# Kernel optimization log

Measured on AMD Instinct MI355X. Metric: run time of the kernel, lower is better.

The kernel has to match this reference:

```python
import jax, jax.numpy as jnp
import numpy as np

B, L, D, M = 4, 8192, 512, 256
EPS = 1e-6


def _feature_map(x, proj, is_query):
    # FAVOR+ positive softmax-kernel features.
    # x: (B, L, D), proj: (M, D) with orthogonal rows scaled by sqrt(D).
    d = x.shape[-1]
    xs = x * (d ** -0.25)                      # scale by d^{-1/4}
    dash = jnp.einsum('bld,md->blm', xs, proj)  # (B, L, M)
    diag = 0.5 * jnp.sum(xs * xs, axis=-1, keepdims=True)  # (B, L, 1)
    if is_query:
        stab = jnp.max(dash, axis=-1, keepdims=True)        # per-position max
    else:
        stab = jnp.max(dash, axis=(-2, -1), keepdims=True)  # per-batch max
    return jnp.exp(dash - diag - stab) / jnp.sqrt(jnp.asarray(M, x.dtype)) + EPS


def setup_inputs() -> dict:
    key = jax.random.key(0)
    kq, kk, kv, kp = jax.random.split(key, 4)
    Q = jax.random.normal(kq, (B, L, D), dtype=jnp.float32)
    K = jax.random.normal(kk, (B, L, D), dtype=jnp.float32)
    V = jax.random.normal(kv, (B, L, D), dtype=jnp.float32)
    # Orthogonal random projection: QR of a Gaussian, rows scaled by sqrt(D).
    G = jax.random.normal(kp, (D, M), dtype=jnp.float32)
    q, _ = jnp.linalg.qr(G)                     # (D, M), orthonormal columns
    proj = q.T * jnp.sqrt(jnp.asarray(D, jnp.float32))  # (M, D)
    return {"Q": Q, "K": K, "V": V, "proj": proj}


def reference(Q, K, V, proj):
    Qf = _feature_map(Q, proj, is_query=True)   # (B, L, M)
    Kf = _feature_map(K, proj, is_query=False)  # (B, L, M)
    # Linear attention: aggregate keys/values once, O(L*M*D).
    KV = jnp.einsum('blm,bld->bmd', Kf, V)      # (B, M, D)
    Ksum = jnp.sum(Kf, axis=1)                  # (B, M)
    Z = 1.0 / (jnp.einsum('blm,bm->bl', Qf, Ksum) + EPS)  # (B, L)
    out = jnp.einsum('blm,bmd->bld', Qf, KV) * Z[..., None]
    return out
```

## Files before the change

### kernel.cpp

```cpp
#include <hip/hip_runtime.h>
#include <math.h>

typedef unsigned short u16;
typedef unsigned int u32;
typedef __attribute__((ext_vector_type(8))) short bf16x8;
typedef __attribute__((ext_vector_type(4))) float f32x4;

#define SCALE_ 0.21022410381342864f
#define EPS_ 1e-6f
#define RSQM_ 0.0625f
#define L_ 8192

__device__ __forceinline__ float bf2f(u16 h) {
    return __uint_as_float(((u32)h) << 16);
}
__device__ __forceinline__ u32 cvtpk(float x0, float x1) {
    u32 w;
    asm("v_cvt_pk_bf16_f32 %0, %1, %2" : "=v"(w) : "v"(x0), "v"(x1));
    return w;
}
__device__ __forceinline__ void split_pk(float x0, float x1, u32& hw, u32& lw) {
    hw = cvtpk(x0, x1);
    float h0 = __uint_as_float(hw << 16);
    float h1 = __uint_as_float(hw & 0xffff0000u);
    lw = cvtpk(x0 - h0, x1 - h1);
}
__device__ __forceinline__ u32 okey(float x) {
    u32 b = __float_as_uint(x);
    return (b & 0x80000000u) ? ~b : (b | 0x80000000u);
}
__device__ __forceinline__ float odec(u32 k) {
    return (k & 0x80000000u) ? __uint_as_float(k & 0x7fffffffu) : __uint_as_float(~k);
}

#define GLDS16(gsrc, ldst) \
    __builtin_amdgcn_global_load_lds((__attribute__((address_space(1))) void*)(gsrc), \
                                     (__attribute__((address_space(3))) void*)(ldst), 16, 0, 0)

__global__ __launch_bounds__(256) void split_p(const float* __restrict__ P,
        u16* __restrict__ Ph, u16* __restrict__ Pl, u32* __restrict__ bmax) {
    if (blockIdx.x == 0 && threadIdx.x < 4) bmax[threadIdx.x] = 0u;
    int i = (blockIdx.x * 256 + threadIdx.x) * 2;
    u32 hw, lw;
    split_pk(P[i] * SCALE_, P[i + 1] * SCALE_, hw, lw);
    *reinterpret_cast<u32*>(&Ph[i]) = hw;
    *reinterpret_cast<u32*>(&Pl[i]) = lw;
}

__global__ __launch_bounds__(256) void dash_all(
        const float* __restrict__ Qg, const float* __restrict__ Kg,
        const u16* __restrict__ Bh_g, const u16* __restrict__ Bl_g,
        u16* __restrict__ QF, u16* __restrict__ KfT, float* __restrict__ ksump,
        u32* __restrict__ bmax) {
    __shared__ __align__(16) u16 Ah[64 * 32], Al[64 * 32];
    __shared__ __align__(16) u16 Bh[256 * 32], Bl[256 * 32];
    const int qpath = !(blockIdx.x & 1);
    const int tile = blockIdx.x >> 1;
    const float* __restrict__ X = qpath ? Qg : Kg;
    const int t = threadIdx.x, lane = t & 63;
    const int wid = t >> 6;
    const int row0 = tile * 64;
    const int l15 = lane & 15, l4 = lane >> 4;
    const int sr = t >> 2;
    const int awz = sr * 32 + (((t & 3) ^ ((sr >> 1) & 3)) * 8);
    const int koff = (l4 ^ ((l15 >> 1) & 3)) * 8;
    float ss = 0.f;

    const float* xp = &X[(size_t)(row0 + sr) * 512 + (t & 3) * 8];
    const u16* bsrch[4];
    const u16* bsrcl[4];
#pragma unroll
    for (int it = 0; it < 4; ++it) {
        const int m = it * 64 + wid * 16 + (lane >> 2);
        const int swz = ((lane & 3) ^ ((m >> 1) & 3)) * 8;
        bsrch[it] = Bh_g + (size_t)m * 512 + swz;
        bsrcl[it] = Bl_g + (size_t)m * 512 + swz;
    }

    f32x4 acc[4][4];
#pragma unroll
    for (int i = 0; i < 4; ++i)
#pragma unroll
        for (int j = 0; j < 4; ++j) acc[i][j] = (f32x4){0.f, 0.f, 0.f, 0.f};

    float4 v0 = *reinterpret_cast<const float4*>(xp);
    float4 v1 = *reinterpret_cast<const float4*>(xp + 4);

    for (int kt = 0; kt < 16; ++kt) {
        __syncthreads();
        {
#pragma unroll
            for (int it = 0; it < 4; ++it) {
                GLDS16(bsrch[it], Bh + it * 2048 + wid * 512);
                GLDS16(bsrcl[it], Bl + it * 2048 + wid * 512);
                bsrch[it] += 32; bsrcl[it] += 32;
            }
            float xs[8] = {v0.x, v0.y, v0.z, v0.w, v1.x, v1.y, v1.z, v1.w};
#pragma unroll
            for (int i = 0; i < 8; ++i) ss = fmaf(xs[i], xs[i], ss);
            u32 hw[4], lw[4];
#pragma unroll
            for (int i = 0; i < 4; ++i) split_pk(xs[2 * i], xs[2 * i + 1], hw[i], lw[i]);
            *reinterpret_cast<uint4*>(&Ah[awz]) = make_uint4(hw[0], hw[1], hw[2], hw[3]);
            *reinterpret_cast<uint4*>(&Al[awz]) = make_uint4(lw[0], lw[1], lw[2], lw[3]);
            xp = (kt < 15) ? xp + 32 : xp;
            v0 = *reinterpret_cast<const float4*>(xp);
            v1 = *reinterpret_cast<const float4*>(xp + 4);
        }
        __syncthreads();
        bf16x8 a_h[4], a_l[4], b_h[4], b_l[4];
#pragma unroll
        for (int mf = 0; mf < 4; ++mf) {
            int r = (mf * 16 + l15) * 32 + koff;
            a_h[mf] = *reinterpret_cast<const bf16x8*>(&Ah[r]);
            a_l[mf] = *reinterpret_cast<const bf16x8*>(&Al[r]);
        }
#pragma unroll
        for (int nf = 0; nf < 4; ++nf) {
            int r = (wid * 64 + nf * 16 + l15) * 32 + koff;
            b_h[nf] = *reinterpret_cast<const bf16x8*>(&Bh[r]);
            b_l[nf] = *reinterpret_cast<const bf16x8*>(&Bl[r]);
        }
#pragma unroll
        for (int mf = 0; mf < 4; ++mf)
#pragma unroll
            for (int nf = 0; nf < 4; ++nf) {
                acc[mf][nf] = __builtin_amdgcn_mfma_f32_16x16x32_bf16(a_h[mf], b_h[nf], acc[mf][nf], 0, 0, 0);
                acc[mf][nf] = __builtin_amdgcn_mfma_f32_16x16x32_bf16(a_h[mf], b_l[nf], acc[mf][nf], 0, 0, 0);
                acc[mf][nf] = __builtin_amdgcn_mfma_f32_16x16x32_bf16(a_l[mf], b_h[nf], acc[mf][nf], 0, 0, 0);
            }
    }
    __syncthreads();
    float* rmaxp = reinterpret_cast<float*>(Ah);
    float* diagp = reinterpret_cast<float*>(Al);

    ss += __shfl_xor(ss, 1);
    ss += __shfl_xor(ss, 2);
    if ((t & 3) == 0) diagp[sr] = 0.5f * SCALE_ * SCALE_ * ss;

    if (qpath) {
        float rm[4][4];
#pragma unroll
        for (int mf = 0; mf < 4; ++mf)
#pragma unroll
            for (int r = 0; r < 4; ++r) {
                float v = fmaxf(fmaxf(acc[mf][0][r], acc[mf][1][r]),
                                fmaxf(acc[mf][2][r], acc[mf][3][r]));
#pragma unroll
                for (int off = 1; off < 16; off <<= 1) v = fmaxf(v, __shfl_xor(v, off));
                rm[mf][r] = v;
            }
        if (l15 == 0) {
#pragma unroll
            for (int mf = 0; mf < 4; ++mf)
#pragma unroll
                for (int r = 0; r < 4; ++r)
                    rmaxp[(mf * 16 + l4 * 4 + r) * 4 + wid] = rm[mf][r];
        }
        __syncthreads();
#pragma unroll
        for (int mf = 0; mf < 4; ++mf)
#pragma unroll
            for (int r = 0; r < 4; ++r) {
                const int rl = mf * 16 + l4 * 4 + r;
                float m4 = fmaxf(fmaxf(rmaxp[rl * 4 + 0], rmaxp[rl * 4 + 1]),
                                 fmaxf(rmaxp[rl * 4 + 2], rmaxp[rl * 4 + 3]));
                const float c = diagp[rl] + m4;
                float f0 = expf(acc[mf][0][r] - c) * RSQM_ + EPS_;
                float f1 = expf(acc[mf][1][r] - c) * RSQM_ + EPS_;
                float f2 = expf(acc[mf][2][r] - c) * RSQM_ + EPS_;
                float f3 = expf(acc[mf][3][r] - c) * RSQM_ + EPS_;
                u32 w01 = cvtpk(f0, f1), w23 = cvtpk(f2, f3);
                size_t o = (size_t)(row0 + rl) * 256 + wid * 64 + l15;
                QF[o]      = (u16)w01;
                QF[o + 16] = (u16)(w01 >> 16);
                QF[o + 32] = (u16)w23;
                QF[o + 48] = (u16)(w23 >> 16);
            }
    } else {
        __syncthreads();
        const int b = row0 >> 13;
        const int ll = row0 & 8191;
        float bm = -1e30f;
        float s[4] = {0.f, 0.f, 0.f, 0.f};
#pragma unroll
        for (int nf = 0; nf < 4; ++nf) {
            const size_t mb = ((size_t)(b * 256 + wid * 64 + nf * 16 + l15)) * 8192 + ll + l4 * 4;
#pragma unroll
            for (int mf = 0; mf < 4; ++mf) {
                float e0 = acc[mf][nf][0], e1 = acc[mf][nf][1];
                float e2 = acc[mf][nf][2], e3 = acc[mf][nf][3];
                bm = fmaxf(fmaxf(bm, fmaxf(e0, e1)), fmaxf(e2, e3));
                float x0 = expf(e0 - diagp[mf * 16 + l4 * 4 + 0]);
                float x1 = expf(e1 - diagp[mf * 16 + l4 * 4 + 1]);
                float x2 = expf(e2 - diagp[mf * 16 + l4 * 4 + 2]);
                float x3 = expf(e3 - diagp[mf * 16 + l4 * 4 + 3]);
                s[nf] += (x0 + x1) + (x2 + x3);
                uint2 w = make_uint2(cvtpk(x0, x1), cvtpk(x2, x3));
                *reinterpret_cast<uint2*>(&KfT[mb + mf * 16]) = w;
            }
        }
#pragma unroll
        for (int nf = 0; nf < 4; ++nf) {
            s[nf] += __shfl_xor(s[nf], 16);
            s[nf] += __shfl_xor(s[nf], 32);
        }
        if (l4 == 0) {
#pragma unroll
            for (int nf = 0; nf < 4; ++nf)
                ksump[tile * 256 + wid * 64 + nf * 16 + l15] = s[nf];
        }
#pragma unroll
        for (int off = 1; off < 64; off <<= 1) bm = fmaxf(bm, __shfl_xor(bm, off));
        if (lane == 0) diagp[64 + wid] = bm;
        __syncthreads();
        if (t == 0) {
            float m = fmaxf(fmaxf(diagp[64], diagp[65]), fmaxf(diagp[66], diagp[67]));
            atomicMax(&bmax[b], okey(m));
        }
    }
}

__global__ __launch_bounds__(256) void split_vt(const float* __restrict__ V,
        u16* __restrict__ Vt, float* __restrict__ vsump) {
    const int dt = blockIdx.x & 7, lt = blockIdx.x >> 3;
    const int lg = lt * 64, b = lg >> 13, d0 = dt * 64;
    __shared__ u16 T[64][72];
    const int t = threadIdx.x;
    const int lrow = t >> 2, c0 = (t & 3) * 16;
#pragma unroll
    for (int ii = 0; ii < 4; ++ii) {
        float4 v = *reinterpret_cast<const float4*>(&V[(size_t)(lg + lrow) * 512 + d0 + c0 + ii * 4]);
        *reinterpret_cast<u32*>(&T[lrow][c0 + ii * 4 + 0]) = cvtpk(v.x, v.y);
        *reinterpret_cast<u32*>(&T[lrow][c0 + ii * 4 + 2]) = cvtpk(v.z, v.w);
    }
    __syncthreads();
    const int dloc = t >> 2, lc = (t & 3) * 16;
    u32 w[8];
    float s = 0.f;
#pragma unroll
    for (int j = 0; j < 8; ++j) {
        u16 a = T[lc + 2 * j][dloc], c = T[lc + 2 * j + 1][dloc];
        w[j] = (u32)a | ((u32)c << 16);
        s += bf2f(a) + bf2f(c);
    }
    size_t ob = ((size_t)(b * 512 + d0 + dloc)) * 8192 + (lg & 8191) + lc;
    reinterpret_cast<uint4*>(&Vt[ob])[0] = make_uint4(w[0], w[1], w[2], w[3]);
    reinterpret_cast<uint4*>(&Vt[ob])[1] = make_uint4(w[4], w[5], w[6], w[7]);
    s += __shfl_xor(s, 1);
    s += __shfl_xor(s, 2);
    if ((t & 3) == 0) vsump[lt * 512 + d0 + dloc] = s;
}

__global__ __launch_bounds__(256) void ksum_red(const float* __restrict__ ksump,
        const u32* __restrict__ bmax, float* __restrict__ KsumT) {
    const int b = blockIdx.x, m = threadIdx.x;
    float s = 0.f;
    for (int j = 0; j < 128; ++j) s += ksump[(b * 128 + j) * 256 + m];
    const float g = expf(-odec(bmax[b]));
    KsumT[b * 256 + m] = g * s + (float)L_ * EPS_;
}

__global__ __launch_bounds__(256) void vsum_red(const float* __restrict__ vsump,
        float* __restrict__ Vsum) {
    const int idx = blockIdx.x * 256 + threadIdx.x;
    const int b = idx >> 9, d = idx & 511;
    float s = 0.f;
    for (int j = 0; j < 128; ++j) s += vsump[(b * 128 + j) * 512 + d];
    Vsum[idx] = s;
}

__global__ __launch_bounds__(256) void kv_mfma(
        const u16* __restrict__ KfT, const u16* __restrict__ Vt,
        float* __restrict__ kvp) {
    int o = (blockIdx.x & 7) * 64 + (blockIdx.x >> 3);
    const int dt = o & 3, mt = (o >> 2) & 1, ch = (o >> 3) & 15, b = o >> 7;
    const u16* Ag = KfT + ((size_t)(b * 256 + mt * 128)) * 8192 + ch * 512;
    const u16* Bg = Vt + ((size_t)(b * 512 + dt * 128)) * 8192 + ch * 512;
    __shared__ __align__(16) u16 A_[128 * 32], B_[128 * 32];
    const int t = threadIdx.x, lane = t & 63;
    const int wid = t >> 6, wr = wid >> 1, wc = wid & 1;
    const int l15 = lane & 15, l4 = lane >> 4;
    const int koff = (l4 ^ ((l15 >> 1) & 3)) * 8;
    const u16* asrc[2];
    const u16* bsrc[2];
#pragma unroll
    for (int it = 0; it < 2; ++it) {
        const int row = it * 64 + wid * 16 + (lane >> 2);
        const int swz = ((lane & 3) ^ ((row >> 1) & 3)) * 8;
        asrc[it] = Ag + (size_t)row * 8192 + swz;
        bsrc[it] = Bg + (size_t)row * 8192 + swz;
    }
    f32x4 acc[4][4];
#pragma unroll
    for (int i = 0; i < 4; ++i)
#pragma unroll
        for (int j = 0; j < 4; ++j) acc[i][j] = (f32x4){0.f, 0.f, 0.f, 0.f};

    for (int kt = 0; kt < 16; ++kt) {
        __syncthreads();
#pragma unroll
        for (int it = 0; it < 2; ++it) {
            GLDS16(asrc[it], A_ + it * 2048 + wid * 512);
            GLDS16(bsrc[it], B_ + it * 2048 + wid * 512);
            asrc[it] += 32; bsrc[it] += 32;
        }
        __syncthreads();
        bf16x8 a[4], bb[4];
#pragma unroll
        for (int mf = 0; mf < 4; ++mf)
            a[mf] = *reinterpret_cast<const bf16x8*>(&A_[(wr * 64 + mf * 16 + l15) * 32 + koff]);
#pragma unroll
        for (int nf = 0; nf < 4; ++nf)
            bb[nf] = *reinterpret_cast<const bf16x8*>(&B_[(wc * 64 + nf * 16 + l15) * 32 + koff]);
#pragma unroll
        for (int mf = 0; mf < 4; ++mf)
#pragma unroll
            for (int nf = 0; nf < 4; ++nf)
                acc[mf][nf] = __builtin_amdgcn_mfma_f32_16x16x32_bf16(a[mf], bb[nf], acc[mf][nf], 0, 0, 0);
    }
#pragma unroll
    for (int mf = 0; mf < 4; ++mf)
#pragma unroll
        for (int r = 0; r < 4; ++r) {
            size_t oo = ((size_t)(ch * 4 + b) * 256 + mt * 128 + wr * 64 + mf * 16 + l4 * 4 + r) * 512
                        + dt * 128 + wc * 64;
#pragma unroll
            for (int nf = 0; nf < 4; ++nf)
                kvp[oo + nf * 16 + l15] = acc[mf][nf][r];
        }
}

__global__ __launch_bounds__(256) void kv_fix(const float* __restrict__ kvp,
        const u32* __restrict__ bmax, const float* __restrict__ Vsum,
        u16* __restrict__ KVth, u16* __restrict__ KVtl) {
    const int dt = blockIdx.x & 7, mt = (blockIdx.x >> 3) & 3, b = blockIdx.x >> 5;
    const int m0 = mt * 64, d0 = dt * 64;
    __shared__ u16 Th[64][72], Tl[64][72];
    const int t = threadIdx.x, mloc = t >> 2, c0 = (t & 3) * 16;
    float s[16];
#pragma unroll
    for (int j = 0; j < 16; ++j) s[j] = 0.f;
    for (int c = 0; c < 16; ++c) {
        size_t base = ((size_t)(c * 4 + b) * 256 + m0 + mloc) * 512 + d0 + c0;
#pragma unroll
        for (int ii = 0; ii < 4; ++ii) {
            float4 v = *reinterpret_cast<const float4*>(&kvp[base + ii * 4]);
            s[ii * 4 + 0] += v.x; s[ii * 4 + 1] += v.y;
            s[ii * 4 + 2] += v.z; s[ii * 4 + 3] += v.w;
        }
    }
    const float g = expf(-odec(bmax[b]));
#pragma unroll
    for (int j = 0; j < 16; j += 2) {
        float v0 = g * s[j]     + EPS_ * Vsum[b * 512 + d0 + c0 + j];
        float v1 = g * s[j + 1] + EPS_ * Vsum[b * 512 + d0 + c0 + j + 1];
        u32 hw, lw; split_pk(v0, v1, hw, lw);
        *reinterpret_cast<u32*>(&Th[mloc][c0 + j]) = hw;
        *reinterpret_cast<u32*>(&Tl[mloc][c0 + j]) = lw;
    }
    __syncthreads();
    const int dloc = t >> 2, mc = (t & 3) * 16;
    size_t ob = ((size_t)(b * 512 + d0 + dloc)) * 256 + m0 + mc;
    u32 wh[8], wl[8];
#pragma unroll
    for (int j = 0; j < 8; ++j) {
        wh[j] = (u32)Th[mc + 2 * j][dloc] | ((u32)Th[mc + 2 * j + 1][dloc] << 16);
        wl[j] = (u32)Tl[mc + 2 * j][dloc] | ((u32)Tl[mc + 2 * j + 1][dloc] << 16);
    }
    reinterpret_cast<uint4*>(&KVth[ob])[0] = make_uint4(wh[0], wh[1], wh[2], wh[3]);
    reinterpret_cast<uint4*>(&KVth[ob])[1] = make_uint4(wh[4], wh[5], wh[6], wh[7]);
    reinterpret_cast<uint4*>(&KVtl[ob])[0] = make_uint4(wl[0], wl[1], wl[2], wl[3]);
    reinterpret_cast<uint4*>(&KVtl[ob])[1] = make_uint4(wl[4], wl[5], wl[6], wl[7]);
}

__global__ __launch_bounds__(256) void z_kernel(const u16* __restrict__ QF,
        const float* __restrict__ KsumT, float* __restrict__ Z) {
    const int wid = threadIdx.x >> 6, lane = threadIdx.x & 63;
    const int row = blockIdx.x * 4 + wid;
    const int b = row >> 13;
    uint2 u = *reinterpret_cast<const uint2*>(&QF[(size_t)row * 256 + lane * 4]);
    float4 ks = *reinterpret_cast<const float4*>(&KsumT[b * 256 + lane * 4]);
    float s = bf2f((u16)(u.x & 0xffff)) * ks.x + bf2f((u16)(u.x >> 16)) * ks.y +
              bf2f((u16)(u.y & 0xffff)) * ks.z + bf2f((u16)(u.y >> 16)) * ks.w;
#pragma unroll
    for (int off = 1; off < 64; off <<= 1) s += __shfl_xor(s, off);
    if (lane == 0) Z[row] = 1.f / (s + EPS_);
}

__global__ __launch_bounds__(256) void out_mfma(
        const u16* __restrict__ QF, const u16* __restrict__ KVth,
        const u16* __restrict__ KVtl, const float* __restrict__ Z,
        float* __restrict__ out) {
    int o = (blockIdx.x & 7) * 128 + (blockIdx.x >> 3);
    const int dt = o & 3, rt = o >> 2;
    const int row0 = rt * 128, b = row0 >> 13;
    const u16* Ag = QF + (size_t)row0 * 256;
    const u16* Bh_g = KVth + ((size_t)(b * 512 + dt * 128)) * 256;
    const u16* Bl_g = KVtl + ((size_t)(b * 512 + dt * 128)) * 256;
    __shared__ __align__(16) u16 A_[128 * 32], Bh_[128 * 32], Bl_[128 * 32];
    const int t = threadIdx.x, lane = t & 63;
    const int wid = t >> 6, wr = wid >> 1, wc = wid & 1;
    const int l15 = lane & 15, l4 = lane >> 4;
    const int koff = (l4 ^ ((l15 >> 1) & 3)) * 8;
    const u16* asrc[2];
    const u16* bhsrc[2];
    const u16* blsrc[2];
#pragma unroll
    for (int it = 0; it < 2; ++it) {
        const int row = it * 64 + wid * 16 + (lane >> 2);
        const int swz = ((lane & 3) ^ ((row >> 1) & 3)) * 8;
        asrc[it]  = Ag + (size_t)row * 256 + swz;
        bhsrc[it] = Bh_g + (size_t)row * 256 + swz;
        blsrc[it] = Bl_g + (size_t)row * 256 + swz;
    }
    f32x4 acc[4][4];
#pragma unroll
    for (int i = 0; i < 4; ++i)
#pragma unroll
        for (int j = 0; j < 4; ++j) acc[i][j] = (f32x4){0.f, 0.f, 0.f, 0.f};

    for (int kt = 0; kt < 8; ++kt) {
        __syncthreads();
#pragma unroll
        for (int it = 0; it < 2; ++it) {
            GLDS16(asrc[it], A_ + it * 2048 + wid * 512);
            GLDS16(bhsrc[it], Bh_ + it * 2048 + wid * 512);
            GLDS16(blsrc[it], Bl_ + it * 2048 + wid * 512);
            asrc[it] += 32; bhsrc[it] += 32; blsrc[it] += 32;
        }
        __syncthreads();
        bf16x8 a[4], bh[4], bl[4];
#pragma unroll
        for (int mf = 0; mf < 4; ++mf)
            a[mf] = *reinterpret_cast<const bf16x8*>(&A_[(wr * 64 + mf * 16 + l15) * 32 + koff]);
#pragma unroll
        for (int nf = 0; nf < 4; ++nf) {
            int r = (wc * 64 + nf * 16 + l15) * 32 + koff;
            bh[nf] = *reinterpret_cast<const bf16x8*>(&Bh_[r]);
            bl[nf] = *reinterpret_cast<const bf16x8*>(&Bl_[r]);
        }
#pragma unroll
        for (int mf = 0; mf < 4; ++mf)
#pragma unroll
            for (int nf = 0; nf < 4; ++nf) {
                acc[mf][nf] = __builtin_amdgcn_mfma_f32_16x16x32_bf16(a[mf], bh[nf], acc[mf][nf], 0, 0, 0);
                acc[mf][nf] = __builtin_amdgcn_mfma_f32_16x16x32_bf16(a[mf], bl[nf], acc[mf][nf], 0, 0, 0);
            }
    }
#pragma unroll
    for (int mf = 0; mf < 4; ++mf)
#pragma unroll
        for (int r = 0; r < 4; ++r) {
            const int row = row0 + wr * 64 + mf * 16 + l4 * 4 + r;
            const float z = Z[row];
#pragma unroll
            for (int nf = 0; nf < 4; ++nf)
                out[(size_t)row * 512 + dt * 128 + wc * 64 + nf * 16 + l15] = acc[mf][nf][r] * z;
        }
}

extern "C" void kernel_launch(void* const* d_in, const int* in_sizes, int n_in,
                              void* d_out, int out_size, void* d_ws, size_t ws_size,
                              hipStream_t stream) {
    const float* Q = (const float*)d_in[0];
    const float* K = (const float*)d_in[1];
    const float* V = (const float*)d_in[2];
    const float* P = (const float*)d_in[3];
    float* out = (float*)d_out;
    char* ws = (char*)d_ws;

    u16*   QF    = (u16*)(ws + 0);
    u16*   KfT   = (u16*)(ws + 16777216);
    u16*   Vt    = (u16*)(ws + 33554432);
    float* kvp   = (float*)(ws + 67108864);
    u16*   KVth  = (u16*)(ws + 100663296);
    u16*   KVtl  = (u16*)(ws + 101711872);
    u16*   PH    = (u16*)(ws + 102760448);
    u16*   PL    = (u16*)(ws + 103022592);
    float* ksump = (float*)(ws + 103284736);
    float* vsump = (float*)(ws + 103809024);
    float* KsumT = (float*)(ws + 104857600);
    float* Vsum  = (float*)(ws + 104861696);
    float* Zbuf  = (float*)(ws + 104869888);
    u32*   bmax  = (u32*)(ws + 105000960);

    split_p<<<256, 256, 0, stream>>>(P, PH, PL, bmax);
    dash_all<<<1024, 256, 0, stream>>>(Q, K, PH, PL, QF, KfT, ksump, bmax);
    split_vt<<<4096, 256, 0, stream>>>(V, Vt, vsump);
    ksum_red<<<4, 256, 0, stream>>>(ksump, bmax, KsumT);
    vsum_red<<<8, 256, 0, stream>>>(vsump, Vsum);
    kv_mfma<<<512, 256, 0, stream>>>(KfT, Vt, kvp);
    kv_fix<<<128, 256, 0, stream>>>(kvp, bmax, Vsum, KVth, KVtl);
    z_kernel<<<8192, 256, 0, stream>>>(QF, KsumT, Zbuf);
    out_mfma<<<1024, 256, 0, stream>>>(QF, KVth, KVtl, Zbuf, out);
}
```

Measured before the change: 174.7 us.

## Fuse V transpose into dash kernel and Z into KV kernel, add setprio

Merges the V-transpose/split kernel into the dash kernel as alternating blocks, and the Z normalizer kernel into the KV MFMA kernel as alternating blocks. This cuts kernel launches and lets memory-bound work overlap with MFMA-bound work. It also fully unrolls the K loops with computed offsets, raises wave priority around the MFMA bursts, and adds occupancy hints to the launch bounds. The kv_mfma loop now shows 16 iterations where a bare label (z_unused) was left in the launch code, which suggests the before excerpt hides part of the context.

```diff
diff --git a/kernel.cpp b/kernel.cpp
--- a/kernel.cpp
+++ b/kernel.cpp
@@ -47,19 +47,59 @@
     *reinterpret_cast<u32*>(&Pl[i]) = lw;
 }
 
-__global__ __launch_bounds__(256) void dash_all(
+__global__ __launch_bounds__(256, 4) void dash_vt(
         const float* __restrict__ Qg, const float* __restrict__ Kg,
+        const float* __restrict__ Vg,
         const u16* __restrict__ Bh_g, const u16* __restrict__ Bl_g,
-        u16* __restrict__ QF, u16* __restrict__ KfT, float* __restrict__ ksump,
+        u16* __restrict__ QF, u16* __restrict__ KfT, u16* __restrict__ Vt,
+        float* __restrict__ ksump, float* __restrict__ vsump,
         u32* __restrict__ bmax) {
     __shared__ __align__(16) u16 Ah[64 * 32], Al[64 * 32];
     __shared__ __align__(16) u16 Bh[256 * 32], Bl[256 * 32];
-    const int qpath = !(blockIdx.x & 1);
-    const int tile = blockIdx.x >> 1;
-    const float* __restrict__ X = qpath ? Qg : Kg;
     const int t = threadIdx.x, lane = t & 63;
     const int wid = t >> 6;
-    const int row0 = tile * 64;
+
+    if (blockIdx.x & 1) {
+        u16 (*T)[72] = reinterpret_cast<u16(*)[72]>(Bh);
+        const int vb = blockIdx.x >> 1;
+        const int lrow = t >> 2, c0 = (t & 3) * 16;
+        const int dloc = t >> 2, lc = (t & 3) * 16;
+        for (int i = 0; i < 4; ++i) {
+            const int tv = vb * 4 + i;
+            const int dt = tv & 7, lt = tv >> 3;
+            const int lg = lt * 64, b = lg >> 13, d0 = dt * 64;
+            __syncthreads();
+#pragma unroll
+            for (int ii = 0; ii < 4; ++ii) {
+                float4 v = *reinterpret_cast<const float4*>(
+                    &Vg[(size_t)(lg + lrow) * 512 + d0 + c0 + ii * 4]);
+                *reinterpret_cast<u32*>(&T[lrow][c0 + ii * 4 + 0]) = cvtpk(v.x, v.y);
+                *reinterpret_cast<u32*>(&T[lrow][c0 + ii * 4 + 2]) = cvtpk(v.z, v.w);
+            }
+            __syncthreads();
+            u32 w[8];
+            float s = 0.f;
+#pragma unroll
+            for (int j = 0; j < 8; ++j) {
+                u16 a = T[lc + 2 * j][dloc], c = T[lc + 2 * j + 1][dloc];
+                w[j] = (u32)a | ((u32)c << 16);
+                s += bf2f(a) + bf2f(c);
+            }
+            size_t ob = ((size_t)(b * 512 + d0 + dloc)) * 8192 + (lg & 8191) + lc;
+            reinterpret_cast<uint4*>(&Vt[ob])[0] = make_uint4(w[0], w[1], w[2], w[3]);
+            reinterpret_cast<uint4*>(&Vt[ob])[1] = make_uint4(w[4], w[5], w[6], w[7]);
+            s += __shfl_xor(s, 1);
+            s += __shfl_xor(s, 2);
+            if ((t & 3) == 0) vsump[lt * 512 + d0 + dloc] = s;
+        }
+        return;
+    }
+
+    const int ds = blockIdx.x >> 1;
+    const int qpath = !(ds & 1);
+    const int xtile = ds >> 1;
+    const float* __restrict__ X = qpath ? Qg : Kg;
+    const int row0 = xtile * 64;
     const int l15 = lane & 15, l4 = lane >> 4;
     const int sr = t >> 2;
     const int awz = sr * 32 + (((t & 3) ^ ((sr >> 1) & 3)) * 8);
@@ -86,14 +126,14 @@
     float4 v0 = *reinterpret_cast<const float4*>(xp);
     float4 v1 = *reinterpret_cast<const float4*>(xp + 4);
 
+#pragma unroll
     for (int kt = 0; kt < 16; ++kt) {
         __syncthreads();
         {
 #pragma unroll
             for (int it = 0; it < 4; ++it) {
-                GLDS16(bsrch[it], Bh + it * 2048 + wid * 512);
-                GLDS16(bsrcl[it], Bl + it * 2048 + wid * 512);
-                bsrch[it] += 32; bsrcl[it] += 32;
+                GLDS16(bsrch[it] + kt * 32, Bh + it * 2048 + wid * 512);
+                GLDS16(bsrcl[it] + kt * 32, Bl + it * 2048 + wid * 512);
             }
             float xs[8] = {v0.x, v0.y, v0.z, v0.w, v1.x, v1.y, v1.z, v1.w};
 #pragma unroll
@@ -103,9 +143,9 @@
             for (int i = 0; i < 4; ++i) split_pk(xs[2 * i], xs[2 * i + 1], hw[i], lw[i]);
             *reinterpret_cast<uint4*>(&Ah[awz]) = make_uint4(hw[0], hw[1], hw[2], hw[3]);
             *reinterpret_cast<uint4*>(&Al[awz]) = make_uint4(lw[0], lw[1], lw[2], lw[3]);
-            xp = (kt < 15) ? xp + 32 : xp;
-            v0 = *reinterpret_cast<const float4*>(xp);
-            v1 = *reinterpret_cast<const float4*>(xp + 4);
+            const int nk = (kt < 15) ? kt + 1 : 15;
+            v0 = *reinterpret_cast<const float4*>(xp + nk * 32);
+            v1 = *reinterpret_cast<const float4*>(xp + nk * 32 + 4);
         }
         __syncthreads();
         bf16x8 a_h[4], a_l[4], b_h[4], b_l[4];
@@ -121,6 +161,7 @@
             b_h[nf] = *reinterpret_cast<const bf16x8*>(&Bh[r]);
             b_l[nf] = *reinterpret_cast<const bf16x8*>(&Bl[r]);
         }
+        __builtin_amdgcn_s_setprio(1);
 #pragma unroll
         for (int mf = 0; mf < 4; ++mf)
 #pragma unroll
@@ -129,6 +170,7 @@
                 acc[mf][nf] = __builtin_amdgcn_mfma_f32_16x16x32_bf16(a_h[mf], b_l[nf], acc[mf][nf], 0, 0, 0);
                 acc[mf][nf] = __builtin_amdgcn_mfma_f32_16x16x32_bf16(a_l[mf], b_h[nf], acc[mf][nf], 0, 0, 0);
             }
+        __builtin_amdgcn_s_setprio(0);
     }
     __syncthreads();
     float* rmaxp = reinterpret_cast<float*>(Ah);
@@ -208,7 +250,7 @@
         if (l4 == 0) {
 #pragma unroll
             for (int nf = 0; nf < 4; ++nf)
-                ksump[tile * 256 + wid * 64 + nf * 16 + l15] = s[nf];
+                ksump[xtile * 256 + wid * 64 + nf * 16 + l15] = s[nf];
         }
 #pragma unroll
         for (int off = 1; off < 64; off <<= 1) bm = fmaxf(bm, __shfl_xor(bm, off));
@@ -219,37 +261,6 @@
             atomicMax(&bmax[b], okey(m));
         }
     }
-}
-
-__global__ __launch_bounds__(256) void split_vt(const float* __restrict__ V,
-        u16* __restrict__ Vt, float* __restrict__ vsump) {
-    const int dt = blockIdx.x & 7, lt = blockIdx.x >> 3;
-    const int lg = lt * 64, b = lg >> 13, d0 = dt * 64;
-    __shared__ u16 T[64][72];
-    const int t = threadIdx.x;
-    const int lrow = t >> 2, c0 = (t & 3) * 16;
-#pragma unroll
-    for (int ii = 0; ii < 4; ++ii) {
-        float4 v = *reinterpret_cast<const float4*>(&V[(size_t)(lg + lrow) * 512 + d0 + c0 + ii * 4]);
-        *reinterpret_cast<u32*>(&T[lrow][c0 + ii * 4 + 0]) = cvtpk(v.x, v.y);
-        *reinterpret_cast<u32*>(&T[lrow][c0 + ii * 4 + 2]) = cvtpk(v.z, v.w);
-    }
-    __syncthreads();
-    const int dloc = t >> 2, lc = (t & 3) * 16;
-    u32 w[8];
-    float s = 0.f;
-#pragma unroll
-    for (int j = 0; j < 8; ++j) {
-        u16 a = T[lc + 2 * j][dloc], c = T[lc + 2 * j + 1][dloc];
-        w[j] = (u32)a | ((u32)c << 16);
-        s += bf2f(a) + bf2f(c);
-    }
-    size_t ob = ((size_t)(b * 512 + d0 + dloc)) * 8192 + (lg & 8191) + lc;
-    reinterpret_cast<uint4*>(&Vt[ob])[0] = make_uint4(w[0], w[1], w[2], w[3]);
-    reinterpret_cast<uint4*>(&Vt[ob])[1] = make_uint4(w[4], w[5], w[6], w[7]);
-    s += __shfl_xor(s, 1);
-    s += __shfl_xor(s, 2);
-    if ((t & 3) == 0) vsump[lt * 512 + d0 + dloc] = s;
 }
 
 __global__ __launch_bounds__(256) void ksum_red(const float* __restrict__ ksump,
@@ -270,16 +281,36 @@
     Vsum[idx] = s;
 }
 
-__global__ __launch_bounds__(256) void kv_mfma(
+__global__ __launch_bounds__(256, 4) void kv_z(
         const u16* __restrict__ KfT, const u16* __restrict__ Vt,
-        float* __restrict__ kvp) {
-    int o = (blockIdx.x & 7) * 64 + (blockIdx.x >> 3);
+        const u16* __restrict__ QF, const float* __restrict__ KsumT,
+        float* __restrict__ kvp, float* __restrict__ Z) {
+    __shared__ __align__(16) u16 A_[128 * 32], B_[128 * 32];
+    const int t = threadIdx.x, lane = t & 63;
+    const int wid = t >> 6;
+
+    if (blockIdx.x & 1) {
+        const int zb = blockIdx.x >> 1;
+        for (int i = 0; i < 16; ++i) {
+            const int row = zb * 64 + wid * 16 + i;
+            const int b = row >> 13;
+            uint2 u = *reinterpret_cast<const uint2*>(&QF[(size_t)row * 256 + lane * 4]);
+            float4 ks = *reinterpret_cast<const float4*>(&KsumT[b * 256 + lane * 4]);
+            float s = bf2f((u16)(u.x & 0xffff)) * ks.x + bf2f((u16)(u.x >> 16)) * ks.y +
+                      bf2f((u16)(u.y & 0xffff)) * ks.z + bf2f((u16)(u.y >> 16)) * ks.w;
+#pragma unroll
+            for (int off = 1; off < 64; off <<= 1) s += __shfl_xor(s, off);
+            if (lane == 0) Z[row] = 1.f / (s + EPS_);
+        }
+        return;
+    }
+
+    const int kvb = blockIdx.x >> 1;
+    int o = (kvb & 7) * 64 + (kvb >> 3);
     const int dt = o & 3, mt = (o >> 2) & 1, ch = (o >> 3) & 15, b = o >> 7;
     const u16* Ag = KfT + ((size_t)(b * 256 + mt * 128)) * 8192 + ch * 512;
     const u16* Bg = Vt + ((size_t)(b * 512 + dt * 128)) * 8192 + ch * 512;
-    __shared__ __align__(16) u16 A_[128 * 32], B_[128 * 32];
-    const int t = threadIdx.x, lane = t & 63;
-    const int wid = t >> 6, wr = wid >> 1, wc = wid & 1;
+    const int wr = wid >> 1, wc = wid & 1;
     const int l15 = lane & 15, l4 = lane >> 4;
     const int koff = (l4 ^ ((l15 >> 1) & 3)) * 8;
     const u16* asrc[2];
@@ -297,13 +328,13 @@
 #pragma unroll
         for (int j = 0; j < 4; ++j) acc[i][j] = (f32x4){0.f, 0.f, 0.f, 0.f};
 
+#pragma unroll
     for (int kt = 0; kt < 16; ++kt) {
         __syncthreads();
 #pragma unroll
         for (int it = 0; it < 2; ++it) {
-            GLDS16(asrc[it], A_ + it * 2048 + wid * 512);
-            GLDS16(bsrc[it], B_ + it * 2048 + wid * 512);
-            asrc[it] += 32; bsrc[it] += 32;
+            GLDS16(asrc[it] + kt * 32, A_ + it * 2048 + wid * 512);
+            GLDS16(bsrc[it] + kt * 32, B_ + it * 2048 + wid * 512);
         }
         __syncthreads();
         bf16x8 a[4], bb[4];
@@ -313,11 +344,13 @@
 #pragma unroll
         for (int nf = 0; nf < 4; ++nf)
             bb[nf] = *reinterpret_cast<const bf16x8*>(&B_[(wc * 64 + nf * 16 + l15) * 32 + koff]);
+        __builtin_amdgcn_s_setprio(1);
 #pragma unroll
         for (int mf = 0; mf < 4; ++mf)
 #pragma unroll
             for (int nf = 0; nf < 4; ++nf)
                 acc[mf][nf] = __builtin_amdgcn_mfma_f32_16x16x32_bf16(a[mf], bb[nf], acc[mf][nf], 0, 0, 0);
+        __builtin_amdgcn_s_setprio(0);
     }
 #pragma unroll
     for (int mf = 0; mf < 4; ++mf)
@@ -374,21 +407,7 @@
     reinterpret_cast<uint4*>(&KVtl[ob])[1] = make_uint4(wl[4], wl[5], wl[6], wl[7]);
 }
 
-__global__ __launch_bounds__(256) void z_kernel(const u16* __restrict__ QF,
-        const float* __restrict__ KsumT, float* __restrict__ Z) {
-    const int wid = threadIdx.x >> 6, lane = threadIdx.x & 63;
-    const int row = blockIdx.x * 4 + wid;
-    const int b = row >> 13;
-    uint2 u = *reinterpret_cast<const uint2*>(&QF[(size_t)row * 256 + lane * 4]);
-    float4 ks = *reinterpret_cast<const float4*>(&KsumT[b * 256 + lane * 4]);
-    float s = bf2f((u16)(u.x & 0xffff)) * ks.x + bf2f((u16)(u.x >> 16)) * ks.y +
-              bf2f((u16)(u.y & 0xffff)) * ks.z + bf2f((u16)(u.y >> 16)) * ks.w;
-#pragma unroll
-    for (int off = 1; off < 64; off <<= 1) s += __shfl_xor(s, off);
-    if (lane == 0) Z[row] = 1.f / (s + EPS_);
-}
-
-__global__ __launch_bounds__(256) void out_mfma(
+__global__ __launch_bounds__(256, 4) void out_mfma(
         const u16* __restrict__ QF, const u16* __restrict__ KVth,
         const u16* __restrict__ KVtl, const float* __restrict__ Z,
         float* __restrict__ out) {
@@ -420,14 +439,14 @@
 #pragma unroll
         for (int j = 0; j < 4; ++j) acc[i][j] = (f32x4){0.f, 0.f, 0.f, 0.f};
 
+#pragma unroll
     for (int kt = 0; kt < 8; ++kt) {
         __syncthreads();
 #pragma unroll
         for (int it = 0; it < 2; ++it) {
-            GLDS16(asrc[it], A_ + it * 2048 + wid * 512);
-            GLDS16(bhsrc[it], Bh_ + it * 2048 + wid * 512);
-            GLDS16(blsrc[it], Bl_ + it * 2048 + wid * 512);
-            asrc[it] += 32; bhsrc[it] += 32; blsrc[it] += 32;
+            GLDS16(asrc[it] + kt * 32, A_ + it * 2048 + wid * 512);
+            GLDS16(bhsrc[it] + kt * 32, Bh_ + it * 2048 + wid * 512);
+            GLDS16(blsrc[it] + kt * 32, Bl_ + it * 2048 + wid * 512);
         }
         __syncthreads();
         bf16x8 a[4], bh[4], bl[4];
@@ -440,6 +459,7 @@
             bh[nf] = *reinterpret_cast<const bf16x8*>(&Bh_[r]);
             bl[nf] = *reinterpret_cast<const bf16x8*>(&Bl_[r]);
         }
+        __builtin_amdgcn_s_setprio(1);
 #pragma unroll
         for (int mf = 0; mf < 4; ++mf)
 #pragma unroll
@@ -447,6 +467,7 @@
                 acc[mf][nf] = __builtin_amdgcn_mfma_f32_16x16x32_bf16(a[mf], bh[nf], acc[mf][nf], 0, 0, 0);
                 acc[mf][nf] = __builtin_amdgcn_mfma_f32_16x16x32_bf16(a[mf], bl[nf], acc[mf][nf], 0, 0, 0);
             }
+        __builtin_amdgcn_s_setprio(0);
     }
 #pragma unroll
     for (int mf = 0; mf < 4; ++mf)
@@ -486,12 +507,11 @@
     u32*   bmax  = (u32*)(ws + 105000960);
 
     split_p<<<256, 256, 0, stream>>>(P, PH, PL, bmax);
-    dash_all<<<1024, 256, 0, stream>>>(Q, K, PH, PL, QF, KfT, ksump, bmax);
-    split_vt<<<4096, 256, 0, stream>>>(V, Vt, vsump);
+    dash_vt<<<2048, 256, 0, stream>>>(Q, K, V, PH, PL, QF, KfT, Vt, ksump, vsump, bmax);
     ksum_red<<<4, 256, 0, stream>>>(ksump, bmax, KsumT);
     vsum_red<<<8, 256, 0, stream>>>(vsump, Vsum);
-    kv_mfma<<<512, 256, 0, stream>>>(KfT, Vt, kvp);
+    kv_z<<<1024, 256, 0, stream>>>(KfT, Vt, QF, KsumT, kvp, Zbuf);
     kv_fix<<<128, 256, 0, stream>>>(kvp, bmax, Vsum, KVth, KVtl);
-    z_kernel<<<8192, 256, 0, stream>>>(QF, KsumT, Zbuf);
+    z_unused:;
     out_mfma<<<1024, 256, 0, stream>>>(QF, KVth, KVtl, Zbuf, out);
 }
```

Result: slower. 593.6 us (+239.8%).
